# Performance work log

Hardware: AMD Instinct MI355X
Metric: run time of the kernel (lower is better)

## Reference

```python
import jax, jax.numpy as jnp
import numpy as np

Q = 10000   # num_question
D = 64      # dim_s
M = 50      # size_m
B = 64      # batch
T = 512     # seq_len


def setup_inputs() -> dict:
    key = jax.random.key(0)
    ks = jax.random.split(key, 14)
    s = 1.0 / np.sqrt(D)
    inp = {
        "question": jax.random.randint(ks[0], (B, T), 0, Q, dtype=jnp.int32),
        "response": jax.random.randint(ks[1], (B, T), 0, 2, dtype=jnp.int32),
        "mask": jnp.ones((B, T), dtype=jnp.float32),
        "k_emb": jax.random.normal(ks[2], (Q, D), jnp.float32) * s,
        "v_emb": jax.random.normal(ks[3], (2 * Q, D), jnp.float32) * s,
        "Mk": jax.random.normal(ks[4], (M, D), jnp.float32) * np.sqrt(2.0 / D),
        "Mv0": jax.random.normal(ks[5], (M, D), jnp.float32) * np.sqrt(2.0 / D),
        "e_W": jax.random.normal(ks[6], (D, D), jnp.float32) * s,
        "e_b": jnp.zeros((D,), jnp.float32),
        "a_W": jax.random.normal(ks[7], (D, D), jnp.float32) * s,
        "a_b": jnp.zeros((D,), jnp.float32),
        "f_W": jax.random.normal(ks[8], (2 * D, D), jnp.float32) * (1.0 / np.sqrt(2 * D)),
        "f_b": jnp.zeros((D,), jnp.float32),
        "p_W": jax.random.normal(ks[9], (D, 1), jnp.float32) * s,
        "p_b": jnp.zeros((1,), jnp.float32),
    }
    return inp


def reference(question, response, mask, k_emb, v_emb, Mk, Mv0,
              e_W, e_b, a_W, a_b, f_W, f_b, p_W, p_b):
    num_q = k_emb.shape[0]
    bsz = question.shape[0]
    x = question + num_q * response                      # [B,T] combined ids
    k = k_emb[question]                                  # [B,T,D]
    v = v_emb[x]                                         # [B,T,D]
    w = jax.nn.softmax(k @ Mk.T, axis=-1)                # [B,T,M] read/write weights
    e = jax.nn.sigmoid(v @ e_W + e_b)                    # [B,T,D] erase
    a = jnp.tanh(v @ a_W + a_b)                          # [B,T,D] add

    def step(Mvt, inp):
        wt, et, at, mt = inp                             # [B,M],[B,D],[B,D],[B]
        Mvn = Mvt * (1.0 - wt[:, :, None] * et[:, None, :]) + wt[:, :, None] * at[:, None, :]
        Mvt = jnp.where(mt[:, None, None] == 1, Mvn, Mvt)
        return Mvt, Mvt

    Mv0b = jnp.broadcast_to(Mv0, (bsz,) + Mv0.shape)     # [B,M,D]
    xs = (jnp.swapaxes(w, 0, 1), jnp.swapaxes(e, 0, 1),
          jnp.swapaxes(a, 0, 1), mask.T)
    _, Mv_seq = jax.lax.scan(step, Mv0b, xs)             # [T,B,M,D] states after steps 0..T-1
    # read at step t (t>=1) uses state after step t-1
    Mv_read = jnp.swapaxes(Mv_seq[:-1], 0, 1)            # [B,T-1,M,D]
    read = jnp.einsum('btm,btmd->btd', w[:, 1:], Mv_read)
    f = jnp.tanh(jnp.concatenate([read, k[:, 1:]], axis=-1) @ f_W + f_b)
    p = (f @ p_W + p_b).squeeze(-1)                      # [B,T-1]
    return p
```

## Files before the change

kernel.cpp:

```cpp
#include <hip/hip_runtime.h>
#include <cstddef>

#define QN 10000
#define DD 64
#define MM 50
#define BB 64
#define TT 512
#define WPAD 52
#define MG 25

__global__ __launch_bounds__(256) void kPre(
    const int* __restrict__ question, const int* __restrict__ response,
    const float* __restrict__ mask,
    const float* __restrict__ k_emb, const float* __restrict__ v_emb,
    const float* __restrict__ Mk,
    const float* __restrict__ e_W, const float* __restrict__ e_b,
    const float* __restrict__ a_W, const float* __restrict__ a_b,
    float* __restrict__ w_buf, float* __restrict__ e_buf,
    float* __restrict__ a_buf) {
  const int lane = (int)(threadIdx.x & 63);
  const int wslot = __builtin_amdgcn_readfirstlane((int)(threadIdx.x >> 6));
  const int gw = blockIdx.x * 4 + wslot;
  const int NW = gridDim.x * 4;
  const int third = NW / 3;

  if (gw < third) {
    float mk[64];
    const int mrow = lane < MM ? lane : (MM - 1);
#pragma unroll
    for (int i = 0; i < 64; i += 4) {
      const float4 t4 = *(const float4*)(Mk + mrow * 64 + i);
      mk[i] = t4.x; mk[i + 1] = t4.y; mk[i + 2] = t4.z; mk[i + 3] = t4.w;
    }
    for (int row = gw; row < BB * TT; row += third) {
      const int q = question[row];
      const float* __restrict__ krow = k_emb + (size_t)q * 64;
      float l0 = 0.f, l1 = 0.f, l2 = 0.f, l3 = 0.f;
#pragma unroll
      for (int i = 0; i < 64; i += 4) {
        const float4 kv = *(const float4*)(krow + i);
        l0 = fmaf(kv.x, mk[i], l0);
        l1 = fmaf(kv.y, mk[i + 1], l1);
        l2 = fmaf(kv.z, mk[i + 2], l2);
        l3 = fmaf(kv.w, mk[i + 3], l3);
      }
      const float lm = (l0 + l1) + (l2 + l3);
      float lv = (lane < MM) ? lm : -3.4e38f;
#pragma unroll
      for (int off = 32; off > 0; off >>= 1) lv = fmaxf(lv, __shfl_xor(lv, off));
      float pe = (lane < MM) ? __expf(lm - lv) : 0.f;
      float ss = pe;
#pragma unroll
      for (int off = 32; off > 0; off >>= 1) ss += __shfl_xor(ss, off);
      if (lane < MM) w_buf[(size_t)row * WPAD + lane] = pe / ss;
    }
  } else if (gw < 2 * third) {
    float ew[64];
#pragma unroll
    for (int i = 0; i < 64; ++i) ew[i] = e_W[i * 64 + lane];
    const float eb = e_b[lane];
    for (int row = gw - third; row < BB * TT; row += third) {
      const int q = question[row];
      const int r = response[row];
      const float mf = (mask[row] == 1.0f) ? 1.0f : 0.0f;
      const float* __restrict__ vrow = v_emb + ((size_t)q + (size_t)QN * r) * 64;
      float e0 = eb, e1 = 0.f;
#pragma unroll
      for (int i = 0; i < 64; i += 2) {
        const float2 vv = *(const float2*)(vrow + i);
        e0 = fmaf(vv.x, ew[i], e0);
        e1 = fmaf(vv.y, ew[i + 1], e1);
      }
      const float se = e0 + e1;
      e_buf[(size_t)row * 64 + lane] = mf / (1.f + __expf(-se));
    }
  } else {
    const int stride = NW - 2 * third;
    float aw[64];
#pragma unroll
    for (int i = 0; i < 64; ++i) aw[i] = a_W[i * 64 + lane];
    const float ab = a_b[lane];
    for (int row = gw - 2 * third; row < BB * TT; row += stride) {
      const int q = question[row];
      const int r = response[row];
      const float mf = (mask[row] == 1.0f) ? 1.0f : 0.0f;
      const float* __restrict__ vrow = v_emb + ((size_t)q + (size_t)QN * r) * 64;
      float a0 = ab, a1 = 0.f;
#pragma unroll
      for (int i = 0; i < 64; i += 2) {
        const float2 vv = *(const float2*)(vrow + i);
        a0 = fmaf(vv.x, aw[i], a0);
        a1 = fmaf(vv.y, aw[i + 1], a1);
      }
      const float sa = a0 + a1;
      const float t2 = __expf(2.f * sa);
      a_buf[(size_t)row * 64 + lane] = mf * (1.f - 2.f / (t2 + 1.f));
    }
  }
}

__global__ __launch_bounds__(256) void kA_chunk(
    const float* __restrict__ w_buf, const float* __restrict__ e_buf,
    const float* __restrict__ a_buf, float* __restrict__ AB, int logC, int L) {
  const int lane = (int)(threadIdx.x & 63);
  const int wslot = __builtin_amdgcn_readfirstlane((int)(threadIdx.x >> 6));
  const int NW = gridDim.x * 4;
  const int C = 1 << logC;
  for (int u2 = blockIdx.x * 4 + wslot; u2 < BB * C * 2; u2 += NW) {
    const int g = u2 & 1;
    const int unit = u2 >> 1;
    const int b = unit >> logC;
    const int c = unit & (C - 1);
    float Am[MG], Bm[MG];
#pragma unroll
    for (int m = 0; m < MG; ++m) { Am[m] = 1.f; Bm[m] = 0.f; }
    const size_t rowbase = (size_t)b * TT + c * L;
#pragma unroll 2
    for (int j = 0; j < L; ++j) {
      const size_t row = rowbase + j;
      const float ed = e_buf[row * 64 + lane];
      const float ad = a_buf[row * 64 + lane];
      const float* __restrict__ wr = w_buf + row * WPAD + g * MG;
#pragma unroll
      for (int m = 0; m < MG; ++m) {
        const float wm = wr[m];
        const float al = fmaf(-wm, ed, 1.0f);
        const float be = wm * ad;
        Am[m] *= al;
        Bm[m] = fmaf(Bm[m], al, be);
      }
    }
    float* __restrict__ abp = AB + (size_t)unit * 6400 + (g * MG) * 128 + lane * 2;
#pragma unroll
    for (int m = 0; m < MG; ++m) {
      float2 o; o.x = Am[m]; o.y = Bm[m];
      *(float2*)(abp + m * 128) = o;
    }
  }
}

__global__ __launch_bounds__(256) void kB_entry(
    const float* __restrict__ AB, const float* __restrict__ Mv0,
    float* __restrict__ entry, int C) {
  const int NT = gridDim.x * 256;
  for (int idx = blockIdx.x * 256 + (int)threadIdx.x; idx < BB * MM * 64;
       idx += NT) {
    const int b = idx / (MM * 64);
    const int r = idx - b * (MM * 64);
    float s = Mv0[r];
    const float* __restrict__ abp = AB + (size_t)b * C * 6400 + (size_t)r * 2;
    float* __restrict__ ep = entry + (size_t)b * C * 3200 + r;
    if (C == 32) {
      float2 ab[32];
#pragma unroll
      for (int c = 0; c < 32; ++c)
        ab[c] = *(const float2*)(abp + (size_t)c * 6400);
#pragma unroll
      for (int c = 0; c < 32; ++c) {
        ep[(size_t)c * 3200] = s;
        s = fmaf(ab[c].x, s, ab[c].y);
      }
    } else {
      float2 cur = *(const float2*)(abp);
      for (int c = 0; c < C; ++c) {
        ep[(size_t)c * 3200] = s;
        float2 nxt; nxt.x = 1.f; nxt.y = 0.f;
        if (c + 1 < C) nxt = *(const float2*)(abp + (size_t)(c + 1) * 6400);
        s = fmaf(cur.x, s, cur.y);
        cur = nxt;
      }
    }
  }
}

__global__ __launch_bounds__(256) void kC_read(
    const float* __restrict__ w_buf, const float* __restrict__ e_buf,
    const float* __restrict__ a_buf, const float* __restrict__ entry,
    const float* __restrict__ Mv0, float* __restrict__ read2,
    int logC, int L, int use_mv0) {
  const int lane = (int)(threadIdx.x & 63);
  const int wslot = __builtin_amdgcn_readfirstlane((int)(threadIdx.x >> 6));
  const int NW = gridDim.x * 4;
  const int C = 1 << logC;
  const size_t RN = (size_t)BB * (TT - 1) * 64;
  for (int u2 = blockIdx.x * 4 + wslot; u2 < BB * C * 2; u2 += NW) {
    const int g = u2 & 1;
    const int unit = u2 >> 1;
    const int b = unit >> logC;
    const int c = unit & (C - 1);

    float s[MG];
    if (use_mv0) {
#pragma unroll
      for (int m = 0; m < MG; ++m) s[m] = Mv0[(g * MG + m) * 64 + lane];
    } else {
      const float* __restrict__ ep =
          entry + (size_t)unit * 3200 + (g * MG) * 64 + lane;
#pragma unroll
      for (int m = 0; m < MG; ++m) s[m] = ep[m * 64];
    }

    const int t0 = c * L;
    float* __restrict__ rb = read2 + (size_t)g * RN;
    int j0 = 0;
    if (t0 == 0) {
      const size_t row = (size_t)b * TT;
      const float ed = e_buf[row * 64 + lane];
      const float ad = a_buf[row * 64 + lane];
      const float* __restrict__ wr = w_buf + row * WPAD + g * MG;
#pragma unroll
      for (int m = 0; m < MG; ++m)
        s[m] = fmaf(wr[m], fmaf(-s[m], ed, ad), s[m]);
      j0 = 1;
    }
#pragma unroll 2
    for (int j = j0; j < L; ++j) {
      const int t = t0 + j;
      const size_t row = (size_t)b * TT + t;
      const float ed = e_buf[row * 64 + lane];
      const float ad = a_buf[row * 64 + lane];
      const float* __restrict__ wr = w_buf + row * WPAD + g * MG;
      float a0 = 0.f, a1 = 0.f;
#pragma unroll
      for (int m = 0; m < MG - 1; m += 2) {
        a0 = fmaf(wr[m], s[m], a0);
        a1 = fmaf(wr[m + 1], s[m + 1], a1);
      }
      a0 = fmaf(wr[MG - 1], s[MG - 1], a0);
      rb[((size_t)b * (TT - 1) + (t - 1)) * 64 + lane] = a0 + a1;
#pragma unroll
      for (int m = 0; m < MG; ++m)
        s[m] = fmaf(wr[m], fmaf(-s[m], ed, ad), s[m]);
    }
  }
}

__global__ __launch_bounds__(256) void k3_out(
    const int* __restrict__ question, const float* __restrict__ k_emb,
    const float* __restrict__ read2,
    const float* __restrict__ f_W, const float* __restrict__ f_b,
    const float* __restrict__ p_W, const float* __restrict__ p_b,
    float* __restrict__ out) {
  const int lane = (int)(threadIdx.x & 63);
  const int wslot = __builtin_amdgcn_readfirstlane((int)(threadIdx.x >> 6));
  const int NW = gridDim.x * 4;
  const size_t RN = (size_t)BB * (TT - 1) * 64;

  float fw[128];
#pragma unroll
  for (int i = 0; i < 128; ++i) fw[i] = f_W[i * 64 + lane];
  const float fb = f_b[lane];
  const float pw = p_W[lane];
  const float pb = p_b[0];

  for (int row = blockIdx.x * 4 + wslot; row < BB * (TT - 1); row += NW) {
    const int b = row / (TT - 1);
    const int tp = row - b * (TT - 1);
    const float* __restrict__ r0 = read2 + (size_t)row * 64;
    const float* __restrict__ r1 = r0 + RN;
    const int qn = question[b * TT + tp + 1];
    const float* __restrict__ krow = k_emb + (size_t)qn * 64;

    float f0 = fb, f1 = 0.f, f2 = 0.f, f3 = 0.f;
#pragma unroll
    for (int i = 0; i < 64; i += 4) {
      const float4 x0 = *(const float4*)(r0 + i);
      const float4 x1 = *(const float4*)(r1 + i);
      f0 = fmaf(x0.x + x1.x, fw[i], f0);
      f1 = fmaf(x0.y + x1.y, fw[i + 1], f1);
      f2 = fmaf(x0.z + x1.z, fw[i + 2], f2);
      f3 = fmaf(x0.w + x1.w, fw[i + 3], f3);
    }
#pragma unroll
    for (int i = 0; i < 64; i += 4) {
      const float4 kv = *(const float4*)(krow + i);
      f0 = fmaf(kv.x, fw[64 + i], f0);
      f1 = fmaf(kv.y, fw[64 + i + 1], f1);
      f2 = fmaf(kv.z, fw[64 + i + 2], f2);
      f3 = fmaf(kv.w, fw[64 + i + 3], f3);
    }
    const float f = (f0 + f1) + (f2 + f3);
    const float t2 = __expf(2.f * f);
    const float fv = 1.f - 2.f / (t2 + 1.f);
    float acc = fv * pw;
#pragma unroll
    for (int off = 32; off > 0; off >>= 1) acc += __shfl_xor(acc, off);
    if (lane == 0) out[row] = acc + pb;
  }
}

extern "C" void kernel_launch(void* const* d_in, const int* in_sizes, int n_in,
                              void* d_out, int out_size, void* d_ws, size_t ws_size,
                              hipStream_t stream) {
  const int*   question = (const int*)d_in[0];
  const int*   response = (const int*)d_in[1];
  const float* mask     = (const float*)d_in[2];
  const float* k_emb    = (const float*)d_in[3];
  const float* v_emb    = (const float*)d_in[4];
  const float* Mk       = (const float*)d_in[5];
  const float* Mv0      = (const float*)d_in[6];
  const float* e_W      = (const float*)d_in[7];
  const float* e_b      = (const float*)d_in[8];
  const float* a_W      = (const float*)d_in[9];
  const float* a_b      = (const float*)d_in[10];
  const float* f_W      = (const float*)d_in[11];
  const float* f_b      = (const float*)d_in[12];
  const float* p_W      = (const float*)d_in[13];
  const float* p_b      = (const float*)d_in[14];
  float* out = (float*)d_out;

  const size_t wN  = (size_t)BB * TT * WPAD;
  const size_t eN  = (size_t)BB * TT * 64;
  const size_t r2N = 2ull * BB * (TT - 1) * 64;
  float* ws = (float*)d_ws;
  float* w_buf  = ws;
  float* e_buf  = w_buf + wN;
  float* a_buf  = e_buf + eN;
  float* read2  = a_buf + eN;
  float* AB_arr = read2 + r2N;
  const size_t baseN = wN + 2 * eN + r2N;

  int C = 32, logC = 5;
  while (C >= 2) {
    const size_t need = (baseN + 9600ull * BB * C) * sizeof(float);
    if (need <= ws_size) break;
    C >>= 1; logC -= 1;
  }
  int useChunks = (C >= 2);
  if (!useChunks) { C = 1; logC = 0; }
  const int L = TT / C;
  float* entry = AB_arr + 6400ull * BB * C;

  hipLaunchKernelGGL(kPre, dim3(2048), dim3(256), 0, stream,
                     question, response, mask, k_emb, v_emb, Mk,
                     e_W, e_b, a_W, a_b, w_buf, e_buf, a_buf);
  if (useChunks) {
    const int ublocksA = (BB * C * 2 + 3) / 4;
    hipLaunchKernelGGL(kA_chunk, dim3(ublocksA), dim3(256), 0, stream,
                       w_buf, e_buf, a_buf, AB_arr, logC, L);
    hipLaunchKernelGGL(kB_entry, dim3((BB * MM * 64 + 255) / 256), dim3(256),
                       0, stream, AB_arr, Mv0, entry, C);
  }
  const int ublocksC = (BB * C * 2 + 3) / 4;
  hipLaunchKernelGGL(kC_read, dim3(ublocksC), dim3(256), 0, stream,
                     w_buf, e_buf, a_buf, entry, Mv0, read2,
                     logC, L, useChunks ? 0 : 1);
  hipLaunchKernelGGL(k3_out, dim3(1024), dim3(256), 0, stream,
                     question, k_emb, read2, f_W, f_b, p_W, p_b, out);
}
```

Baseline: 212.8 us.

## Batch four rows per wave in preprocessing and specialize chunked scan for C=32

The preprocessing kernel now has each wave handle four consecutive rows at once, with vector loads of question, response and mask and four independent accumulator chains. This raises memory-level parallelism and amortizes the per-row index loads. For the default C=32 case it adds fully unrolled chunk-summary and read kernels (kA16, kC16) with a compile-time length of 16. These preload the e and a vectors into registers and drop the loop-trip overheads. Register pressure rises from the extra accumulators and preloaded arrays, which could lower occupancy.

Result: no change. 211.4 us (-0.6%).

```diff
diff --git a/kernel.cpp b/kernel.cpp
--- a/kernel.cpp
+++ b/kernel.cpp
@@ -23,8 +23,12 @@
   const int gw = blockIdx.x * 4 + wslot;
   const int NW = gridDim.x * 4;
   const int third = NW / 3;
-
-  if (gw < third) {
+  if (gw >= 3 * third) return;
+  const int role = gw / third;
+  const int idx = gw - role * third;
+  const int stride4 = third * 4;
+
+  if (role == 0) {
     float mk[64];
     const int mrow = lane < MM ? lane : (MM - 1);
 #pragma unroll
@@ -32,70 +36,251 @@
       const float4 t4 = *(const float4*)(Mk + mrow * 64 + i);
       mk[i] = t4.x; mk[i + 1] = t4.y; mk[i + 2] = t4.z; mk[i + 3] = t4.w;
     }
-    for (int row = gw; row < BB * TT; row += third) {
-      const int q = question[row];
-      const float* __restrict__ krow = k_emb + (size_t)q * 64;
-      float l0 = 0.f, l1 = 0.f, l2 = 0.f, l3 = 0.f;
+    for (int base = idx * 4; base < BB * TT; base += stride4) {
+      const int4 q4 = *(const int4*)(question + base);
+      const float* __restrict__ kr0 = k_emb + (size_t)q4.x * 64;
+      const float* __restrict__ kr1 = k_emb + (size_t)q4.y * 64;
+      const float* __restrict__ kr2 = k_emb + (size_t)q4.z * 64;
+      const float* __restrict__ kr3 = k_emb + (size_t)q4.w * 64;
+      float l00=0.f,l01=0.f,l02=0.f,l03=0.f;
+      float l10=0.f,l11=0.f,l12=0.f,l13=0.f;
+      float l20=0.f,l21=0.f,l22=0.f,l23=0.f;
+      float l30=0.f,l31=0.f,l32=0.f,l33=0.f;
 #pragma unroll
       for (int i = 0; i < 64; i += 4) {
-        const float4 kv = *(const float4*)(krow + i);
-        l0 = fmaf(kv.x, mk[i], l0);
-        l1 = fmaf(kv.y, mk[i + 1], l1);
-        l2 = fmaf(kv.z, mk[i + 2], l2);
-        l3 = fmaf(kv.w, mk[i + 3], l3);
-      }
-      const float lm = (l0 + l1) + (l2 + l3);
-      float lv = (lane < MM) ? lm : -3.4e38f;
-#pragma unroll
-      for (int off = 32; off > 0; off >>= 1) lv = fmaxf(lv, __shfl_xor(lv, off));
-      float pe = (lane < MM) ? __expf(lm - lv) : 0.f;
-      float ss = pe;
-#pragma unroll
-      for (int off = 32; off > 0; off >>= 1) ss += __shfl_xor(ss, off);
-      if (lane < MM) w_buf[(size_t)row * WPAD + lane] = pe / ss;
-    }
-  } else if (gw < 2 * third) {
+        const float4 k0 = *(const float4*)(kr0 + i);
+        const float4 k1 = *(const float4*)(kr1 + i);
+        const float4 k2 = *(const float4*)(kr2 + i);
+        const float4 k3 = *(const float4*)(kr3 + i);
+        l00 = fmaf(k0.x, mk[i], l00); l01 = fmaf(k0.y, mk[i+1], l01);
+        l02 = fmaf(k0.z, mk[i+2], l02); l03 = fmaf(k0.w, mk[i+3], l03);
+        l10 = fmaf(k1.x, mk[i], l10); l11 = fmaf(k1.y, mk[i+1], l11);
+        l12 = fmaf(k1.z, mk[i+2], l12); l13 = fmaf(k1.w, mk[i+3], l13);
+        l20 = fmaf(k2.x, mk[i], l20); l21 = fmaf(k2.y, mk[i+1], l21);
+        l22 = fmaf(k2.z, mk[i+2], l22); l23 = fmaf(k2.w, mk[i+3], l23);
+        l30 = fmaf(k3.x, mk[i], l30); l31 = fmaf(k3.y, mk[i+1], l31);
+        l32 = fmaf(k3.z, mk[i+2], l32); l33 = fmaf(k3.w, mk[i+3], l33);
+      }
+      float lm[4];
+      lm[0] = (l00 + l01) + (l02 + l03);
+      lm[1] = (l10 + l11) + (l12 + l13);
+      lm[2] = (l20 + l21) + (l22 + l23);
+      lm[3] = (l30 + l31) + (l32 + l33);
+#pragma unroll
+      for (int r = 0; r < 4; ++r) {
+        float lv = (lane < MM) ? lm[r] : -3.4e38f;
+#pragma unroll
+        for (int off = 32; off > 0; off >>= 1) lv = fmaxf(lv, __shfl_xor(lv, off));
+        float pe = (lane < MM) ? __expf(lm[r] - lv) : 0.f;
+        float ss = pe;
+#pragma unroll
+        for (int off = 32; off > 0; off >>= 1) ss += __shfl_xor(ss, off);
+        if (lane < MM) w_buf[(size_t)(base + r) * WPAD + lane] = pe / ss;
+      }
+    }
+  } else if (role == 1) {
     float ew[64];
 #pragma unroll
     for (int i = 0; i < 64; ++i) ew[i] = e_W[i * 64 + lane];
     const float eb = e_b[lane];
-    for (int row = gw - third; row < BB * TT; row += third) {
-      const int q = question[row];
-      const int r = response[row];
-      const float mf = (mask[row] == 1.0f) ? 1.0f : 0.0f;
-      const float* __restrict__ vrow = v_emb + ((size_t)q + (size_t)QN * r) * 64;
-      float e0 = eb, e1 = 0.f;
+    for (int base = idx * 4; base < BB * TT; base += stride4) {
+      const int4 q4 = *(const int4*)(question + base);
+      const int4 r4 = *(const int4*)(response + base);
+      const float4 m4 = *(const float4*)(mask + base);
+      const float* __restrict__ v0 = v_emb + ((size_t)q4.x + (size_t)QN * r4.x) * 64;
+      const float* __restrict__ v1 = v_emb + ((size_t)q4.y + (size_t)QN * r4.y) * 64;
+      const float* __restrict__ v2 = v_emb + ((size_t)q4.z + (size_t)QN * r4.z) * 64;
+      const float* __restrict__ v3 = v_emb + ((size_t)q4.w + (size_t)QN * r4.w) * 64;
+      float e00 = eb, e01 = 0.f, e10 = eb, e11 = 0.f;
+      float e20 = eb, e21 = 0.f, e30 = eb, e31 = 0.f;
 #pragma unroll
       for (int i = 0; i < 64; i += 2) {
-        const float2 vv = *(const float2*)(vrow + i);
-        e0 = fmaf(vv.x, ew[i], e0);
-        e1 = fmaf(vv.y, ew[i + 1], e1);
-      }
-      const float se = e0 + e1;
-      e_buf[(size_t)row * 64 + lane] = mf / (1.f + __expf(-se));
+        const float2 a0 = *(const float2*)(v0 + i);
+        const float2 a1 = *(const float2*)(v1 + i);
+        const float2 a2 = *(const float2*)(v2 + i);
+        const float2 a3 = *(const float2*)(v3 + i);
+        e00 = fmaf(a0.x, ew[i], e00); e01 = fmaf(a0.y, ew[i+1], e01);
+        e10 = fmaf(a1.x, ew[i], e10); e11 = fmaf(a1.y, ew[i+1], e11);
+        e20 = fmaf(a2.x, ew[i], e20); e21 = fmaf(a2.y, ew[i+1], e21);
+        e30 = fmaf(a3.x, ew[i], e30); e31 = fmaf(a3.y, ew[i+1], e31);
+      }
+      const float mf0 = (m4.x == 1.0f) ? 1.0f : 0.0f;
+      const float mf1 = (m4.y == 1.0f) ? 1.0f : 0.0f;
+      const float mf2 = (m4.z == 1.0f) ? 1.0f : 0.0f;
+      const float mf3 = (m4.w == 1.0f) ? 1.0f : 0.0f;
+      e_buf[(size_t)(base + 0) * 64 + lane] = mf0 / (1.f + __expf(-(e00 + e01)));
+      e_buf[(size_t)(base + 1) * 64 + lane] = mf1 / (1.f + __expf(-(e10 + e11)));
+      e_buf[(size_t)(base + 2) * 64 + lane] = mf2 / (1.f + __expf(-(e20 + e21)));
+      e_buf[(size_t)(base + 3) * 64 + lane] = mf3 / (1.f + __expf(-(e30 + e31)));
     }
   } else {
-    const int stride = NW - 2 * third;
     float aw[64];
 #pragma unroll
     for (int i = 0; i < 64; ++i) aw[i] = a_W[i * 64 + lane];
     const float ab = a_b[lane];
-    for (int row = gw - 2 * third; row < BB * TT; row += stride) {
-      const int q = question[row];
-      const int r = response[row];
-      const float mf = (mask[row] == 1.0f) ? 1.0f : 0.0f;
-      const float* __restrict__ vrow = v_emb + ((size_t)q + (size_t)QN * r) * 64;
-      float a0 = ab, a1 = 0.f;
+    for (int base = idx * 4; base < BB * TT; base += stride4) {
+      const int4 q4 = *(const int4*)(question + base);
+      const int4 r4 = *(const int4*)(response + base);
+      const float4 m4 = *(const float4*)(mask + base);
+      const float* __restrict__ v0 = v_emb + ((size_t)q4.x + (size_t)QN * r4.x) * 64;
+      const float* __restrict__ v1 = v_emb + ((size_t)q4.y + (size_t)QN * r4.y) * 64;
+      const float* __restrict__ v2 = v_emb + ((size_t)q4.z + (size_t)QN * r4.z) * 64;
+      const float* __restrict__ v3 = v_emb + ((size_t)q4.w + (size_t)QN * r4.w) * 64;
+      float a00 = ab, a01 = 0.f, a10 = ab, a11 = 0.f;
+      float a20 = ab, a21 = 0.f, a30 = ab, a31 = 0.f;
 #pragma unroll
       for (int i = 0; i < 64; i += 2) {
-        const float2 vv = *(const float2*)(vrow + i);
-        a0 = fmaf(vv.x, aw[i], a0);
-        a1 = fmaf(vv.y, aw[i + 1], a1);
-      }
-      const float sa = a0 + a1;
-      const float t2 = __expf(2.f * sa);
-      a_buf[(size_t)row * 64 + lane] = mf * (1.f - 2.f / (t2 + 1.f));
-    }
+        const float2 x0 = *(const float2*)(v0 + i);
+        const float2 x1 = *(const float2*)(v1 + i);
+        const float2 x2 = *(const float2*)(v2 + i);
+        const float2 x3 = *(const float2*)(v3 + i);
+        a00 = fmaf(x0.x, aw[i], a00); a01 = fmaf(x0.y, aw[i+1], a01);
+        a10 = fmaf(x1.x, aw[i], a10); a11 = fmaf(x1.y, aw[i+1], a11);
+        a20 = fmaf(x2.x, aw[i], a20); a21 = fmaf(x2.y, aw[i+1], a21);
+        a30 = fmaf(x3.x, aw[i], a30); a31 = fmaf(x3.y, aw[i+1], a31);
+      }
+      const float mf0 = (m4.x == 1.0f) ? 1.0f : 0.0f;
+      const float mf1 = (m4.y == 1.0f) ? 1.0f : 0.0f;
+      const float mf2 = (m4.z == 1.0f) ? 1.0f : 0.0f;
+      const float mf3 = (m4.w == 1.0f) ? 1.0f : 0.0f;
+      const float s0 = a00 + a01, s1 = a10 + a11, s2 = a20 + a21, s3 = a30 + a31;
+      a_buf[(size_t)(base + 0) * 64 + lane] = mf0 * (1.f - 2.f / (__expf(2.f * s0) + 1.f));
+      a_buf[(size_t)(base + 1) * 64 + lane] = mf1 * (1.f - 2.f / (__expf(2.f * s1) + 1.f));
+      a_buf[(size_t)(base + 2) * 64 + lane] = mf2 * (1.f - 2.f / (__expf(2.f * s2) + 1.f));
+      a_buf[(size_t)(base + 3) * 64 + lane] = mf3 * (1.f - 2.f / (__expf(2.f * s3) + 1.f));
+    }
+  }
+}
+
+__global__ __launch_bounds__(256) void kA16(
+    const float* __restrict__ w_buf, const float* __restrict__ e_buf,
+    const float* __restrict__ a_buf, float* __restrict__ AB) {
+  const int lane = (int)(threadIdx.x & 63);
+  const int wslot = __builtin_amdgcn_readfirstlane((int)(threadIdx.x >> 6));
+  const int u2 = blockIdx.x * 4 + wslot;
+  if (u2 >= BB * 32 * 2) return;
+  const int g = u2 & 1;
+  const int unit = u2 >> 1;
+  const int b = unit >> 5;
+  const int c = unit & 31;
+  const size_t rowbase = (size_t)b * TT + c * 16;
+  const size_t eb0 = rowbase * 64 + lane;
+
+  float ev[16], av[16];
+#pragma unroll
+  for (int j = 0; j < 16; ++j) {
+    ev[j] = e_buf[eb0 + (size_t)j * 64];
+    av[j] = a_buf[eb0 + (size_t)j * 64];
+  }
+
+  float Am[MG], Bm[MG];
+#pragma unroll
+  for (int m = 0; m < MG; ++m) { Am[m] = 1.f; Bm[m] = 0.f; }
+
+#pragma unroll
+  for (int j = 0; j < 16; ++j) {
+    const float* __restrict__ wr = w_buf + (rowbase + j) * WPAD + g * MG;
+#pragma unroll
+    for (int m = 0; m < MG; ++m) {
+      const float wm = wr[m];
+      const float al = fmaf(-wm, ev[j], 1.0f);
+      const float be = wm * av[j];
+      Am[m] *= al;
+      Bm[m] = fmaf(Bm[m], al, be);
+    }
+  }
+  float* __restrict__ abp = AB + (size_t)unit * 6400 + (g * MG) * 128 + lane * 2;
+#pragma unroll
+  for (int m = 0; m < MG; ++m) {
+    float2 o; o.x = Am[m]; o.y = Bm[m];
+    *(float2*)(abp + m * 128) = o;
+  }
+}
+
+__global__ __launch_bounds__(256) void kB_entry(
+    const float* __restrict__ AB, const float* __restrict__ Mv0,
+    float* __restrict__ entry, int C) {
+  const int NT = gridDim.x * 256;
+  for (int idx = blockIdx.x * 256 + (int)threadIdx.x; idx < BB * MM * 64;
+       idx += NT) {
+    const int b = idx / (MM * 64);
+    const int r = idx - b * (MM * 64);
+    float s = Mv0[r];
+    const float* __restrict__ abp = AB + (size_t)b * C * 6400 + (size_t)r * 2;
+    float* __restrict__ ep = entry + (size_t)b * C * 3200 + r;
+    if (C == 32) {
+      float2 ab[32];
+#pragma unroll
+      for (int c = 0; c < 32; ++c)
+        ab[c] = *(const float2*)(abp + (size_t)c * 6400);
+#pragma unroll
+      for (int c = 0; c < 32; ++c) {
+        ep[(size_t)c * 3200] = s;
+        s = fmaf(ab[c].x, s, ab[c].y);
+      }
+    } else {
+      float2 cur = *(const float2*)(abp);
+      for (int c = 0; c < C; ++c) {
+        ep[(size_t)c * 3200] = s;
+        float2 nxt; nxt.x = 1.f; nxt.y = 0.f;
+        if (c + 1 < C) nxt = *(const float2*)(abp + (size_t)(c + 1) * 6400);
+        s = fmaf(cur.x, s, cur.y);
+        cur = nxt;
+      }
+    }
+  }
+}
+
+__global__ __launch_bounds__(256) void kC16(
+    const float* __restrict__ w_buf, const float* __restrict__ e_buf,
+    const float* __restrict__ a_buf, const float* __restrict__ entry,
+    float* __restrict__ read2) {
+  const int lane = (int)(threadIdx.x & 63);
+  const int wslot = __builtin_amdgcn_readfirstlane((int)(threadIdx.x >> 6));
+  const int u2 = blockIdx.x * 4 + wslot;
+  if (u2 >= BB * 32 * 2) return;
+  const int g = u2 & 1;
+  const int unit = u2 >> 1;
+  const int b = unit >> 5;
+  const int c = unit & 31;
+  const size_t RN = (size_t)BB * (TT - 1) * 64;
+  const size_t rowbase = (size_t)b * TT + c * 16;
+  const size_t eb0 = rowbase * 64 + lane;
+
+  float ev[16], av[16];
+#pragma unroll
+  for (int j = 0; j < 16; ++j) {
+    ev[j] = e_buf[eb0 + (size_t)j * 64];
+    av[j] = a_buf[eb0 + (size_t)j * 64];
+  }
+
+  float s[MG];
+  {
+    const float* __restrict__ ep =
+        entry + (size_t)unit * 3200 + (g * MG) * 64 + lane;
+#pragma unroll
+    for (int m = 0; m < MG; ++m) s[m] = ep[m * 64];
+  }
+
+  const int t0 = c * 16;
+  float* __restrict__ rb = read2 + (size_t)g * RN;
+#pragma unroll
+  for (int j = 0; j < 16; ++j) {
+    const int t = t0 + j;
+    const float* __restrict__ wr = w_buf + (rowbase + j) * WPAD + g * MG;
+    if (t >= 1) {
+      float a0 = 0.f, a1 = 0.f;
+#pragma unroll
+      for (int m = 0; m < MG - 1; m += 2) {
+        a0 = fmaf(wr[m], s[m], a0);
+        a1 = fmaf(wr[m + 1], s[m + 1], a1);
+      }
+      a0 = fmaf(wr[MG - 1], s[MG - 1], a0);
+      rb[((size_t)b * (TT - 1) + (t - 1)) * 64 + lane] = a0 + a1;
+    }
+#pragma unroll
+    for (int m = 0; m < MG; ++m)
+      s[m] = fmaf(wr[m], fmaf(-s[m], ev[j], av[j]), s[m]);
   }
 }
 
@@ -135,40 +320,6 @@
     for (int m = 0; m < MG; ++m) {
       float2 o; o.x = Am[m]; o.y = Bm[m];
       *(float2*)(abp + m * 128) = o;
-    }
-  }
-}
-
-__global__ __launch_bounds__(256) void kB_entry(
-    const float* __restrict__ AB, const float* __restrict__ Mv0,
-    float* __restrict__ entry, int C) {
-  const int NT = gridDim.x * 256;
-  for (int idx = blockIdx.x * 256 + (int)threadIdx.x; idx < BB * MM * 64;
-       idx += NT) {
-    const int b = idx / (MM * 64);
-    const int r = idx - b * (MM * 64);
-    float s = Mv0[r];
-    const float* __restrict__ abp = AB + (size_t)b * C * 6400 + (size_t)r * 2;
-    float* __restrict__ ep = entry + (size_t)b * C * 3200 + r;
-    if (C == 32) {
-      float2 ab[32];
-#pragma unroll
-      for (int c = 0; c < 32; ++c)
-        ab[c] = *(const float2*)(abp + (size_t)c * 6400);
-#pragma unroll
-      for (int c = 0; c < 32; ++c) {
-        ep[(size_t)c * 3200] = s;
-        s = fmaf(ab[c].x, s, ab[c].y);
-      }
-    } else {
-      float2 cur = *(const float2*)(abp);
-      for (int c = 0; c < C; ++c) {
-        ep[(size_t)c * 3200] = s;
-        float2 nxt; nxt.x = 1.f; nxt.y = 0.f;
-        if (c + 1 < C) nxt = *(const float2*)(abp + (size_t)(c + 1) * 6400);
-        s = fmaf(cur.x, s, cur.y);
-        cur = nxt;
-      }
     }
   }
 }
@@ -188,7 +339,6 @@
     const int unit = u2 >> 1;
     const int b = unit >> logC;
     const int c = unit & (C - 1);
-
     float s[MG];
     if (use_mv0) {
 #pragma unroll
@@ -199,35 +349,24 @@
 #pragma unroll
       for (int m = 0; m < MG; ++m) s[m] = ep[m * 64];
     }
-
     const int t0 = c * L;
     float* __restrict__ rb = read2 + (size_t)g * RN;
-    int j0 = 0;
-    if (t0 == 0) {
-      const size_t row = (size_t)b * TT;
-      const float ed = e_buf[row * 64 + lane];
-      const float ad = a_buf[row * 64 + lane];
-      const float* __restrict__ wr = w_buf + row * WPAD + g * MG;
-#pragma unroll
-      for (int m = 0; m < MG; ++m)
-        s[m] = fmaf(wr[m], fmaf(-s[m], ed, ad), s[m]);
-      j0 = 1;
-    }
-#pragma unroll 2
-    for (int j = j0; j < L; ++j) {
+    for (int j = 0; j < L; ++j) {
       const int t = t0 + j;
       const size_t row = (size_t)b * TT + t;
       const float ed = e_buf[row * 64 + lane];
       const float ad = a_buf[row * 64 + lane];
       const float* __restrict__ wr = w_buf + row * WPAD + g * MG;
-      float a0 = 0.f, a1 = 0.f;
-#pragma unroll
-      for (int m = 0; m < MG - 1; m += 2) {
-        a0 = fmaf(wr[m], s[m], a0);
-        a1 = fmaf(wr[m + 1], s[m + 1], a1);
-      }
-      a0 = fmaf(wr[MG - 1], s[MG - 1], a0);
-      rb[((size_t)b * (TT - 1) + (t - 1)) * 64 + lane] = a0 + a1;
+      if (t >= 1) {
+        float a0 = 0.f, a1 = 0.f;
+#pragma unroll
+        for (int m = 0; m < MG - 1; m += 2) {
+          a0 = fmaf(wr[m], s[m], a0);
+          a1 = fmaf(wr[m + 1], s[m + 1], a1);
+        }
+        a0 = fmaf(wr[MG - 1], s[MG - 1], a0);
+        rb[((size_t)b * (TT - 1) + (t - 1)) * 64 + lane] = a0 + a1;
+      }
 #pragma unroll
       for (int m = 0; m < MG; ++m)
         s[m] = fmaf(wr[m], fmaf(-s[m], ed, ad), s[m]);
@@ -334,17 +473,28 @@
   hipLaunchKernelGGL(kPre, dim3(2048), dim3(256), 0, stream,
                      question, response, mask, k_emb, v_emb, Mk,
                      e_W, e_b, a_W, a_b, w_buf, e_buf, a_buf);
-  if (useChunks) {
-    const int ublocksA = (BB * C * 2 + 3) / 4;
-    hipLaunchKernelGGL(kA_chunk, dim3(ublocksA), dim3(256), 0, stream,
-                       w_buf, e_buf, a_buf, AB_arr, logC, L);
+
+  if (C == 32) {
+    hipLaunchKernelGGL(kA16, dim3(1024), dim3(256), 0, stream,
+                       w_buf, e_buf, a_buf, AB_arr);
     hipLaunchKernelGGL(kB_entry, dim3((BB * MM * 64 + 255) / 256), dim3(256),
                        0, stream, AB_arr, Mv0, entry, C);
-  }
-  const int ublocksC = (BB * C * 2 + 3) / 4;
-  hipLaunchKernelGGL(kC_read, dim3(ublocksC), dim3(256), 0, stream,
-                     w_buf, e_buf, a_buf, entry, Mv0, read2,
-                     logC, L, useChunks ? 0 : 1);
+    hipLaunchKernelGGL(kC16, dim3(1024), dim3(256), 0, stream,
+                       w_buf, e_buf, a_buf, entry, read2);
+  } else {
+    if (useChunks) {
+      const int ublocksA = (BB * C * 2 + 3) / 4;
+      hipLaunchKernelGGL(kA_chunk, dim3(ublocksA), dim3(256), 0, stream,
+                         w_buf, e_buf, a_buf, AB_arr, logC, L);
+      hipLaunchKernelGGL(kB_entry, dim3((BB * MM * 64 + 255) / 256), dim3(256),
+                         0, stream, AB_arr, Mv0, entry, C);
+    }
+    const int ublocksC = (BB * C * 2 + 3) / 4;
+    hipLaunchKernelGGL(kC_read, dim3(ublocksC), dim3(256), 0, stream,
+                       w_buf, e_buf, a_buf, entry, Mv0, read2,
+                       logC, L, useChunks ? 0 : 1);
+  }
+
   hipLaunchKernelGGL(k3_out, dim3(1024), dim3(256), 0, stream,
                      question, k_emb, read2, f_W, f_b, p_W, p_b, out);
 }
```
